# Performance work log

Measured on AMD Instinct MI355X. Metric: run time of the kernel, lower is better.

## Reference

```python
import jax, jax.numpy as jnp
import numpy as np

# SwitchNet f* dims
B = 1024
Nb1, Nw1 = 8, 10          # input: Nb1^2=64 blocks, window 2*Nw1^2=200
Nb2x, Nb2y = 8, 8
Nw2x, Nw2y = 10, 10
R = 16
J1 = Nb1 * Nb1            # 64
K1 = 2 * Nw1 * Nw1        # 200
L1 = Nb2x * Nb2y * R      # 1024
J2 = Nb2x * Nb2y * J1     # 4096
J3 = Nb2x * Nb2y          # 64
K3 = J1 * R               # 1024
L3 = 2 * Nw2x * Nw2y      # 200


def _dm(x, kernel, bias):
    # per-block batched GEMM: x [B, J, K] @ kernel [J, K, L] + bias [1, J, L]
    return jnp.einsum('ijk,jkl->ijl', x, kernel) + bias


def setup_inputs() -> dict:
    key = jax.random.key(0)
    ks = jax.random.split(key, 7)
    u = lambda k, shape: jax.random.uniform(k, shape, dtype=jnp.float32) * 0.01
    return {
        'x': jax.random.normal(ks[0], (B, Nb1 * Nw1 * Nb1 * Nw1, 2), dtype=jnp.float32),
        'k1': u(ks[1], (J1, K1, L1)),
        'b1': u(ks[2], (1, J1, L1)),
        'k2': u(ks[3], (J2, R, R)),
        'b2': u(ks[4], (1, J2, R)),
        'k3': u(ks[5], (J3, K3, L3)),
        'b3': u(ks[6], (1, J3, L3)),
    }


def reference(x, k1, b1, k2, b2, k3, b3):
    bs = x.shape[0]
    # gather input windows: [B, Nb1, Nw1, Nb1, Nw1, 2] -> block-major
    h = x.reshape(bs, Nb1, Nw1, Nb1, Nw1, 2)
    h = h.transpose(0, 1, 3, 2, 4, 5)
    h = h.reshape(bs, J1, K1)
    h = _dm(h, k1, b1)                                   # [B, 64, 1024]
    h = h.reshape(bs, J1, Nb2x * Nb2y, R)
    h = h.transpose(0, 3, 1, 2)                          # [B, r, 64, 64]
    h = h.reshape(bs, J2, R)
    h = _dm(h, k2, b2)                                   # [B, 4096, r]
    h = h.reshape(bs, J3, K3)
    h = _dm(h, k3, b3)                                   # [B, 64, 200]
    h = h.reshape(bs, Nb2x, Nb2y, Nw2x, Nw2y, 2)
    h = h.transpose(0, 1, 3, 2, 4, 5)
    return h.reshape(bs, Nb2x * Nw2x, Nb2y * Nw2y, 2)   # [B, 80, 80, 2]
```

## Files before the change

### kernel.cpp

```cpp
#include <hip/hip_runtime.h>

typedef __attribute__((ext_vector_type(8))) short short8;
typedef __attribute__((ext_vector_type(4))) short bfx4;
typedef __attribute__((ext_vector_type(4))) float floatx4;

__device__ __forceinline__ float bf2f(short u) {
  unsigned int i = ((unsigned int)(unsigned short)u) << 16;
  return __builtin_bit_cast(float, i);
}
__device__ __forceinline__ short f2bf(float f) {
  unsigned int x = __builtin_bit_cast(unsigned int, f);
  x += 0x7fffu + ((x >> 16) & 1u);
  return (short)(x >> 16);
}

__device__ __forceinline__ void gl_lds16(const short* g, short* lds) {
  __builtin_amdgcn_global_load_lds(
      (const __attribute__((address_space(1))) unsigned int*)g,
      (__attribute__((address_space(3))) unsigned int*)lds, 16, 0, 0);
}

#define BC 256


__global__ __launch_bounds__(256) void gather_x(const float* __restrict__ x,
                                                short* __restrict__ hA, int bOffset) {
  int tid = blockIdx.x * 256 + threadIdx.x;
  const int total = 64 * BC * 112;
  if (tid >= total) return;
  int kp2 = tid % 112;
  int rem = tid / 112;
  int b_loc = rem & (BC - 1);
  int j1 = rem / BC;
  unsigned int pair = 0;
  if (kp2 < 100) {
    int wx = kp2 / 10;
    int wy = kp2 - wx * 10;
    int bx = j1 >> 3, by = j1 & 7;
    const float* p = x + (size_t)(bOffset + b_loc) * 12800 +
                     ((size_t)(bx * 800 + wx * 80 + by * 10 + wy)) * 2;
    float2 v = *(const float2*)p;
    pair = ((unsigned int)(unsigned short)f2bf(v.x)) |
           (((unsigned int)(unsigned short)f2bf(v.y)) << 16);
  }
  *(unsigned int*)&hA[rem * 224 + kp2 * 2] = pair;
}

__global__ __launch_bounds__(256) void transpose_k1(const float* __restrict__ k1,
                                                    short* __restrict__ k1t) {
  const int j1 = blockIdx.x;
  const int nBase = blockIdx.y * 64;
  const int kBase = blockIdx.z * 56;
  __shared__ short tr[64][68];
  const int t = threadIdx.x;
  const int nl = t & 63;
  const int ksub = t >> 6;
  const float* src = k1 + (size_t)j1 * 204800 + (size_t)kBase * 1024 + nBase + nl;
#pragma unroll
  for (int pass = 0; pass < 14; ++pass) {
    int kloc = pass * 4 + ksub;
    int k = kBase + kloc;
    tr[nl][kloc] = (k < 200) ? f2bf(src[kloc * 1024]) : (short)0;
  }
  __syncthreads();
  short* dstbase = k1t + ((size_t)j1 * 1024 + nBase) * 224 + kBase;
#pragma unroll
  for (int p = 0; p < 4; ++p) {
    int u = p * 256 + t;
    int row = u >> 4;
    int kq = u & 15;
    if (kq < 14) {
      bfx4 v = *(const bfx4*)&tr[row][kq * 4];
      *(bfx4*)&dstbase[row * 224 + kq * 4] = v;
    }
  }
}

__global__ __launch_bounds__(256) void transpose_k3(const float* __restrict__ k3,
                                                    short* __restrict__ k3t) {
  const int j3 = blockIdx.x;
  const int kBase = blockIdx.y * 128;
  const int nBase = blockIdx.z * 64;
  __shared__ short tr[64][132];
  const int t = threadIdx.x;
  const int nl = t & 63;
  const int ksub = t >> 6;
  const int nGlob = nBase + nl;
  const bool valid = (nGlob < 200);
  const float* src = k3 + (size_t)j3 * 204800 + (size_t)kBase * 200 + nGlob;
#pragma unroll 4
  for (int pass = 0; pass < 32; ++pass) {
    int k = pass * 4 + ksub;
    tr[nl][k] = valid ? f2bf(src[k * 200]) : (short)0;
  }
  __syncthreads();
  short* dstbase = k3t + ((size_t)j3 * 256 + nBase) * 1024 + kBase;
#pragma unroll
  for (int pass = 0; pass < 8; ++pass) {
    int idx = (pass * 256 + t) * 4;
    int row = idx >> 7;
    int koff = idx & 127;
    bfx4 v = *(const bfx4*)&tr[row][koff];
    *(bfx4*)&dstbase[row * 1024 + koff] = v;
  }
}

__global__ __launch_bounds__(256) void gemm_stage1(const short* __restrict__ hA,
                                                   const short* __restrict__ k1t,
                                                   const float* __restrict__ b1,
                                                   short* __restrict__ h1) {
  int bid = (int)blockIdx.x + 8 * (int)blockIdx.y + 16 * (int)blockIdx.z;
  bid = ((bid & 7) << 7) | (bid >> 3);
  const int nBase = (bid & 7) * 128;
  const int mBase = ((bid >> 3) & 1) * 128;
  const int j1 = bid >> 4;
  __shared__ short As[128 * 64];
  __shared__ short Bs[128 * 64];
  const int tid = threadIdx.x;
  const int lane = tid & 63;
  const int wave = tid >> 6;
  const int quad = lane >> 4;
  const int l16 = lane & 15;
  const int wm = wave >> 1, wn = wave & 1;
  const int sRow = tid >> 3;
  const int sCol = ((tid & 7) ^ (sRow & 7)) * 8;
  const short* Aj = hA + (size_t)j1 * BC * 224 + (size_t)(mBase + sRow) * 224 + sCol;
  const short* Bj =
      k1t + (size_t)j1 * 1024 * 224 + (size_t)(nBase + sRow) * 224 + sCol;
  const int tRow = tid >> 2;
  const int tCol = (tid & 3) * 8;
  const short* Ajt =
      hA + (size_t)j1 * BC * 224 + (size_t)(mBase + tRow) * 224 + 192 + tCol;
  const short* Bjt =
      k1t + (size_t)j1 * 1024 * 224 + (size_t)(nBase + tRow) * 224 + 192 + tCol;
  short* ldsA = &As[tid * 8];
  short* ldsB = &Bs[tid * 8];
  floatx4 acc[4][4] = {};

  for (int kk = 0; kk < 192; kk += 64) {
    __syncthreads();
#pragma unroll
    for (int c = 0; c < 4; ++c) {
      gl_lds16(Aj + c * 32 * 224 + kk, ldsA + c * 2048);
      gl_lds16(Bj + c * 32 * 224 + kk, ldsB + c * 2048);
    }
    __syncthreads();
#pragma unroll
    for (int ks = 0; ks < 2; ++ks) {
      short8 af[4], bfv[4];
#pragma unroll
      for (int mt = 0; mt < 4; ++mt) {
        int r = wm * 64 + mt * 16 + l16;
        af[mt] = *(const short8*)&As[r * 64 + ((ks * 4 + quad) ^ (l16 & 7)) * 8];
      }
#pragma unroll
      for (int nt = 0; nt < 4; ++nt) {
        int r = wn * 64 + nt * 16 + l16;
        bfv[nt] = *(const short8*)&Bs[r * 64 + ((ks * 4 + quad) ^ (l16 & 7)) * 8];
      }
#pragma unroll
      for (int mt = 0; mt < 4; ++mt)
#pragma unroll
        for (int nt = 0; nt < 4; ++nt)
          acc[mt][nt] = __builtin_amdgcn_mfma_f32_16x16x32_bf16(af[mt], bfv[nt],
                                                                acc[mt][nt], 0, 0, 0);
    }
  }
  __syncthreads();
  gl_lds16(Ajt, ldsA);
  gl_lds16(Ajt + 64 * 224, ldsA + 2048);
  gl_lds16(Bjt, ldsB);
  gl_lds16(Bjt + 64 * 224, ldsB + 2048);
  __syncthreads();
  {
    short8 af[4], bfv[4];
#pragma unroll
    for (int mt = 0; mt < 4; ++mt)
      af[mt] = *(const short8*)&As[(wm * 64 + mt * 16 + l16) * 32 + quad * 8];
#pragma unroll
    for (int nt = 0; nt < 4; ++nt)
      bfv[nt] = *(const short8*)&Bs[(wn * 64 + nt * 16 + l16) * 32 + quad * 8];
#pragma unroll
    for (int mt = 0; mt < 4; ++mt)
#pragma unroll
      for (int nt = 0; nt < 4; ++nt)
        acc[mt][nt] = __builtin_amdgcn_mfma_f32_16x16x32_bf16(af[mt], bfv[nt],
                                                              acc[mt][nt], 0, 0, 0);
  }
#pragma unroll
  for (int nt = 0; nt < 4; ++nt) {
    int n = nBase + wn * 64 + nt * 16 + l16;
    float bias = b1[j1 * 1024 + n];
    int g = (nBase + wn * 64 + nt * 16) >> 4;
    int nst = ((((g & 15) << 2) | (g >> 4)) << 4) + l16;
#pragma unroll
    for (int mt = 0; mt < 4; ++mt) {
#pragma unroll
      for (int r = 0; r < 4; ++r) {
        int m = mBase + wm * 64 + mt * 16 + quad * 4 + r;
        h1[((size_t)j1 * BC + m) * 1024 + nst] = f2bf(acc[mt][nt][r] + bias);
      }
    }
  }
}

__global__ __launch_bounds__(256) void stage2(const short* __restrict__ h1,
                                              const float* __restrict__ k2,
                                              const float* __restrict__ b2,
                                              short* __restrict__ h2p, int mTot,
                                              int bOff2) {
  int bid = (int)blockIdx.x + 64 * (int)blockIdx.y;
  bid = ((bid & 7) << 7) | (bid >> 3);
  const int j1 = bid >> 4;
  const int bBase = (bid & 15) * 16;
  __shared__ short in_s[16 * 1024];
  const int tid = threadIdx.x;

  const short* inSrc = h1 + ((size_t)j1 * BC + bBase) * 1024 + tid * 8;
  short* inDst = &in_s[tid * 8];
#pragma unroll
  for (int c = 0; c < 8; ++c) gl_lds16(inSrc + c * 2048, inDst + c * 2048);

  const int rem = tid & 63;
  const int oct = tid >> 6;
  const int bh = oct & 1;
  const int ro = oct >> 1;
  const int r = rem >> 2, b2hi = rem & 3;
  const int j2 = r * 256 + j1 * 4 + b2hi;

  float acc[8][8];
  {
    const float* bb = &b2[(size_t)j2 * 16 + ro * 8];
    floatx4 bz0 = *(const floatx4*)bb;
    floatx4 bz1 = *(const floatx4*)(bb + 4);
#pragma unroll
    for (int b = 0; b < 8; ++b)
#pragma unroll
      for (int j = 0; j < 4; ++j) {
        acc[b][j] = bz0[j];
        acc[b][4 + j] = bz1[j];
      }
  }
  __syncthreads();

  const short* inb = &in_s[(bh * 8) * 1024 + b2hi * 16 + r];
  const float* wsrc = &k2[(size_t)j2 * 256 + ro * 8];
#pragma unroll
  for (int k = 0; k < 16; ++k) {
    floatx4 w0 = *(const floatx4*)&wsrc[k * 16];
    floatx4 w1 = *(const floatx4*)&wsrc[k * 16 + 4];
#pragma unroll
    for (int b = 0; b < 8; ++b) {
      float iv = bf2f(inb[b * 1024 + k * 64]);
#pragma unroll
      for (int j = 0; j < 4; ++j) {
        acc[b][j] += iv * w0[j];
        acc[b][4 + j] += iv * w1[j];
      }
    }
  }
  const int j3 = r * 4 + (j1 >> 4);
  const int k3o = (j1 & 15) * 64 + b2hi * 16 + ro * 8;
#pragma unroll
  for (int b = 0; b < 8; ++b) {
    short8 o;
#pragma unroll
    for (int j = 0; j < 8; ++j) o[j] = f2bf(acc[b][j]);
    short* dst =
        h2p + ((size_t)j3 * mTot + bOff2 + bBase + bh * 8 + b) * 1024 + k3o;
    *(short8*)dst = o;
  }
}

__global__ __launch_bounds__(256) void gemm_stage3(const short* __restrict__ h2p,
                                                   const short* __restrict__ k3t,
                                                   const float* __restrict__ b3,
                                                   float* __restrict__ out, int mTot,
                                                   int bOffset) {
  const int gy = (int)gridDim.y;
  int bid = (int)blockIdx.x + 2 * ((int)blockIdx.y + gy * (int)blockIdx.z);
  const int cpx = (gy << 4);
  bid = (bid & 7) * cpx + (bid >> 3);
  const int nBase = (bid & 1) * 128;
  const int rest = bid >> 1;
  const int mBase = (rest & (gy - 1)) * 128;
  const int j3 = rest / gy;
  __shared__ short As[128 * 64];
  __shared__ short Bs[128 * 64];
  const int tid = threadIdx.x;
  const int lane = tid & 63;
  const int wave = tid >> 6;
  const int quad = lane >> 4;
  const int l16 = lane & 15;
  const int wm = wave >> 1, wn = wave & 1;
  const int sRow = tid >> 3;
  const int sCol = ((tid & 7) ^ (sRow & 7)) * 8;
  const short* Aj =
      h2p + (size_t)j3 * mTot * 1024 + (size_t)(mBase + sRow) * 1024 + sCol;
  const short* Bj =
      k3t + (size_t)j3 * 256 * 1024 + (size_t)(nBase + sRow) * 1024 + sCol;
  short* ldsA = &As[tid * 8];
  short* ldsB = &Bs[tid * 8];
  floatx4 acc[4][4] = {};

  for (int kk = 0; kk < 1024; kk += 64) {
    __syncthreads();
#pragma unroll
    for (int c = 0; c < 4; ++c) {
      gl_lds16(Aj + c * 32 * 1024 + kk, ldsA + c * 2048);
      gl_lds16(Bj + c * 32 * 1024 + kk, ldsB + c * 2048);
    }
    __syncthreads();
#pragma unroll
    for (int ks = 0; ks < 2; ++ks) {
      short8 af[4], bfv[4];
#pragma unroll
      for (int mt = 0; mt < 4; ++mt) {
        int r = wm * 64 + mt * 16 + l16;
        af[mt] = *(const short8*)&As[r * 64 + ((ks * 4 + quad) ^ (l16 & 7)) * 8];
      }
#pragma unroll
      for (int nt = 0; nt < 4; ++nt) {
        int r = wn * 64 + nt * 16 + l16;
        bfv[nt] = *(const short8*)&Bs[r * 64 + ((ks * 4 + quad) ^ (l16 & 7)) * 8];
      }
#pragma unroll
      for (int mt = 0; mt < 4; ++mt)
#pragma unroll
        for (int nt = 0; nt < 4; ++nt)
          acc[mt][nt] = __builtin_amdgcn_mfma_f32_16x16x32_bf16(af[mt], bfv[nt],
                                                                acc[mt][nt], 0, 0, 0);
    }
  }
  const int B2x = j3 >> 3, B2y = j3 & 7;
#pragma unroll
  for (int nt = 0; nt < 4; ++nt) {
    int n = nBase + wn * 64 + nt * 16 + l16;
    if (n < 200) {
      float bias = b3[j3 * 200 + n];
      int c = n & 1;
      int t = n >> 1;
      int w2x = t / 10, w2y = t - w2x * 10;
      int orow = B2x * 10 + w2x, ocol = B2y * 10 + w2y;
#pragma unroll
      for (int mt = 0; mt < 4; ++mt) {
#pragma unroll
        for (int r = 0; r < 4; ++r) {
          int m = bOffset + mBase + wm * 64 + mt * 16 + quad * 4 + r;
          out[(((size_t)m * 80 + orow) * 80 + ocol) * 2 + c] = acc[mt][nt][r] + bias;
        }
      }
    }
  }
}

extern "C" void kernel_launch(void* const* d_in, const int* in_sizes, int n_in,
                              void* d_out, int out_size, void* d_ws, size_t ws_size,
                              hipStream_t stream) {
  const float* x = (const float*)d_in[0];
  const float* k1 = (const float*)d_in[1];
  const float* b1 = (const float*)d_in[2];
  const float* k2 = (const float*)d_in[3];
  const float* b2 = (const float*)d_in[4];
  const float* k3 = (const float*)d_in[5];
  const float* b3 = (const float*)d_in[6];
  float* out = (float*)d_out;
  char* ws = (char*)d_ws;

  short* k1t = (short*)(ws);
  short* k3t = (short*)(ws + 29360128);
  short* hA = (short*)(ws + 62914560);
  short* h1c = (short*)(ws + 70254592);
  short* h2p = (short*)(ws + 103809024);

  const bool full = (ws_size >= 238026752ull);
  const int mTot = full ? 1024 : BC;

  transpose_k1<<<dim3(64, 16, 4), 256, 0, stream>>>(k1, k1t);
  transpose_k3<<<dim3(64, 8, 4), 256, 0, stream>>>(k3, k3t);
  for (int c = 0; c < 1024 / BC; ++c) {
    int bOffset = c * BC;
    gather_x<<<(64 * BC * 112) / 256, 256, 0, stream>>>(x, hA, bOffset);
    gemm_stage1<<<dim3(8, BC / 128, 64), 256, 0, stream>>>(hA, k1t, b1, h1c);
    stage2<<<dim3(64, BC / 16), 256, 0, stream>>>(h1c, k2, b2, h2p, mTot,
                                                  full ? bOffset : 0);
    if (!full)
      gemm_stage3<<<dim3(2, BC / 128, 64), 256, 0, stream>>>(h2p, k3t, b3, out, BC,
                                                             bOffset);
  }
  if (full)
    gemm_stage3<<<dim3(2, 1024 / 128, 64), 256, 0, stream>>>(h2p, k3t, b3, out, 1024,
                                                             0);
}
```

Before: 488.0 us.

## Fuse stage-1 GEMM with stage-2 block mixing through shared memory

New measurement: 506.9 us. 3.9% more time.

```diff
diff --git a/kernel.cpp b/kernel.cpp
--- a/kernel.cpp
+++ b/kernel.cpp
@@ -20,18 +20,16 @@
       (__attribute__((address_space(3))) unsigned int*)lds, 16, 0, 0);
 }
 
-#define BC 256
-
-
 __global__ __launch_bounds__(256) void gather_x(const float* __restrict__ x,
-                                                short* __restrict__ hA, int bOffset) {
+                                                short* __restrict__ hA, int bOffset,
+                                                int bShift) {
   int tid = blockIdx.x * 256 + threadIdx.x;
-  const int total = 64 * BC * 112;
+  const int total = (64 << bShift) * 116;
   if (tid >= total) return;
-  int kp2 = tid % 112;
-  int rem = tid / 112;
-  int b_loc = rem & (BC - 1);
-  int j1 = rem / BC;
+  int kp2 = tid % 116;
+  int rem = tid / 116;
+  int b_loc = rem & ((1 << bShift) - 1);
+  int j1 = rem >> bShift;
   unsigned int pair = 0;
   if (kp2 < 100) {
     int wx = kp2 / 10;
@@ -43,7 +41,7 @@
     pair = ((unsigned int)(unsigned short)f2bf(v.x)) |
            (((unsigned int)(unsigned short)f2bf(v.y)) << 16);
   }
-  *(unsigned int*)&hA[rem * 224 + kp2 * 2] = pair;
+  *(unsigned int*)&hA[(size_t)rem * 232 + kp2 * 2] = pair;
 }
 
 __global__ __launch_bounds__(256) void transpose_k1(const float* __restrict__ k1,
@@ -105,170 +103,160 @@
   }
 }
 
-__global__ __launch_bounds__(256) void gemm_stage1(const short* __restrict__ hA,
-                                                   const short* __restrict__ k1t,
-                                                   const float* __restrict__ b1,
-                                                   short* __restrict__ h1) {
-  int bid = (int)blockIdx.x + 8 * (int)blockIdx.y + 16 * (int)blockIdx.z;
-  bid = ((bid & 7) << 7) | (bid >> 3);
-  const int nBase = (bid & 7) * 128;
-  const int mBase = ((bid >> 3) & 1) * 128;
-  const int j1 = bid >> 4;
-  __shared__ short As[128 * 64];
-  __shared__ short Bs[128 * 64];
+__global__ __launch_bounds__(256) void fused12(
+    const short* __restrict__ hA, const short* __restrict__ k1t,
+    const float* __restrict__ b1, const float* __restrict__ k2,
+    const float* __restrict__ b2, short* __restrict__ h2p, int h2pTot,
+    int h2pOff) {
+  const int gx = (int)gridDim.x;
+  int bid = (int)blockIdx.x + gx * (int)blockIdx.y;
+  const int cpx = gx * 8;
+  bid = (bid & 7) * cpx + (bid >> 3);
+  const int j1 = bid / gx;
+  const int mt = bid - j1 * gx;
+  const int BCc = gx * 64;
+
+  __shared__ short lds[31488];
+  short* As = lds;
+  short* Bs = lds + 14848;
+  short* Cs = lds + 23040;
+
   const int tid = threadIdx.x;
   const int lane = tid & 63;
   const int wave = tid >> 6;
   const int quad = lane >> 4;
   const int l16 = lane & 15;
   const int wm = wave >> 1, wn = wave & 1;
+
+  {
+    const short* Asrc = hA + ((size_t)j1 * BCc + mt * 64) * 232 + tid * 8;
+    short* Adst = As + tid * 8;
+#pragma unroll
+    for (int c = 0; c < 8; ++c) gl_lds16(Asrc + c * 2048, Adst + c * 2048);
+  }
+
   const int sRow = tid >> 3;
   const int sCol = ((tid & 7) ^ (sRow & 7)) * 8;
-  const short* Aj = hA + (size_t)j1 * BC * 224 + (size_t)(mBase + sRow) * 224 + sCol;
-  const short* Bj =
-      k1t + (size_t)j1 * 1024 * 224 + (size_t)(nBase + sRow) * 224 + sCol;
+  const short* BjS = k1t + (size_t)j1 * 1024 * 224 + (size_t)sRow * 224 + sCol;
   const int tRow = tid >> 2;
   const int tCol = (tid & 3) * 8;
-  const short* Ajt =
-      hA + (size_t)j1 * BC * 224 + (size_t)(mBase + tRow) * 224 + 192 + tCol;
-  const short* Bjt =
-      k1t + (size_t)j1 * 1024 * 224 + (size_t)(nBase + tRow) * 224 + 192 + tCol;
-  short* ldsA = &As[tid * 8];
+  const short* BjT =
+      k1t + (size_t)j1 * 1024 * 224 + (size_t)tRow * 224 + 192 + tCol;
   short* ldsB = &Bs[tid * 8];
-  floatx4 acc[4][4] = {};
-
-  for (int kk = 0; kk < 192; kk += 64) {
-    __syncthreads();
-#pragma unroll
-    for (int c = 0; c < 4; ++c) {
-      gl_lds16(Aj + c * 32 * 224 + kk, ldsA + c * 2048);
-      gl_lds16(Bj + c * 32 * 224 + kk, ldsB + c * 2048);
-    }
-    __syncthreads();
-#pragma unroll
-    for (int ks = 0; ks < 2; ++ks) {
-      short8 af[4], bfv[4];
-#pragma unroll
-      for (int mt = 0; mt < 4; ++mt) {
-        int r = wm * 64 + mt * 16 + l16;
-        af[mt] = *(const short8*)&As[r * 64 + ((ks * 4 + quad) ^ (l16 & 7)) * 8];
-      }
-#pragma unroll
-      for (int nt = 0; nt < 4; ++nt) {
-        int r = wn * 64 + nt * 16 + l16;
-        bfv[nt] = *(const short8*)&Bs[r * 64 + ((ks * 4 + quad) ^ (l16 & 7)) * 8];
-      }
-#pragma unroll
-      for (int mt = 0; mt < 4; ++mt)
-#pragma unroll
-        for (int nt = 0; nt < 4; ++nt)
-          acc[mt][nt] = __builtin_amdgcn_mfma_f32_16x16x32_bf16(af[mt], bfv[nt],
-                                                                acc[mt][nt], 0, 0, 0);
-    }
-  }
-  __syncthreads();
-  gl_lds16(Ajt, ldsA);
-  gl_lds16(Ajt + 64 * 224, ldsA + 2048);
-  gl_lds16(Bjt, ldsB);
-  gl_lds16(Bjt + 64 * 224, ldsB + 2048);
-  __syncthreads();
-  {
-    short8 af[4], bfv[4];
-#pragma unroll
-    for (int mt = 0; mt < 4; ++mt)
-      af[mt] = *(const short8*)&As[(wm * 64 + mt * 16 + l16) * 32 + quad * 8];
-#pragma unroll
-    for (int nt = 0; nt < 4; ++nt)
-      bfv[nt] = *(const short8*)&Bs[(wn * 64 + nt * 16 + l16) * 32 + quad * 8];
-#pragma unroll
-    for (int mt = 0; mt < 4; ++mt)
-#pragma unroll
-      for (int nt = 0; nt < 4; ++nt)
-        acc[mt][nt] = __builtin_amdgcn_mfma_f32_16x16x32_bf16(af[mt], bfv[nt],
-                                                              acc[mt][nt], 0, 0, 0);
-  }
-#pragma unroll
-  for (int nt = 0; nt < 4; ++nt) {
-    int n = nBase + wn * 64 + nt * 16 + l16;
-    float bias = b1[j1 * 1024 + n];
-    int g = (nBase + wn * 64 + nt * 16) >> 4;
-    int nst = ((((g & 15) << 2) | (g >> 4)) << 4) + l16;
-#pragma unroll
-    for (int mt = 0; mt < 4; ++mt) {
-#pragma unroll
-      for (int r = 0; r < 4; ++r) {
-        int m = mBase + wm * 64 + mt * 16 + quad * 4 + r;
-        h1[((size_t)j1 * BC + m) * 1024 + nst] = f2bf(acc[mt][nt][r] + bias);
-      }
-    }
-  }
-}
-
-__global__ __launch_bounds__(256) void stage2(const short* __restrict__ h1,
-                                              const float* __restrict__ k2,
-                                              const float* __restrict__ b2,
-                                              short* __restrict__ h2p, int mTot,
-                                              int bOff2) {
-  int bid = (int)blockIdx.x + 64 * (int)blockIdx.y;
-  bid = ((bid & 7) << 7) | (bid >> 3);
-  const int j1 = bid >> 4;
-  const int bBase = (bid & 15) * 16;
-  __shared__ short in_s[16 * 1024];
-  const int tid = threadIdx.x;
-
-  const short* inSrc = h1 + ((size_t)j1 * BC + bBase) * 1024 + tid * 8;
-  short* inDst = &in_s[tid * 8];
-#pragma unroll
-  for (int c = 0; c < 8; ++c) gl_lds16(inSrc + c * 2048, inDst + c * 2048);
-
-  const int rem = tid & 63;
-  const int oct = tid >> 6;
-  const int bh = oct & 1;
-  const int ro = oct >> 1;
-  const int r = rem >> 2, b2hi = rem & 3;
-  const int j2 = r * 256 + j1 * 4 + b2hi;
-
-  float acc[8][8];
-  {
-    const float* bb = &b2[(size_t)j2 * 16 + ro * 8];
-    floatx4 bz0 = *(const floatx4*)bb;
-    floatx4 bz1 = *(const floatx4*)(bb + 4);
-#pragma unroll
-    for (int b = 0; b < 8; ++b)
-#pragma unroll
-      for (int j = 0; j < 4; ++j) {
-        acc[b][j] = bz0[j];
-        acc[b][4 + j] = bz1[j];
-      }
-  }
-  __syncthreads();
-
-  const short* inb = &in_s[(bh * 8) * 1024 + b2hi * 16 + r];
-  const float* wsrc = &k2[(size_t)j2 * 256 + ro * 8];
-#pragma unroll
-  for (int k = 0; k < 16; ++k) {
-    floatx4 w0 = *(const floatx4*)&wsrc[k * 16];
-    floatx4 w1 = *(const floatx4*)&wsrc[k * 16 + 4];
-#pragma unroll
-    for (int b = 0; b < 8; ++b) {
-      float iv = bf2f(inb[b * 1024 + k * 64]);
-#pragma unroll
-      for (int j = 0; j < 4; ++j) {
-        acc[b][j] += iv * w0[j];
-        acc[b][4 + j] += iv * w1[j];
-      }
-    }
-  }
-  const int j3 = r * 4 + (j1 >> 4);
-  const int k3o = (j1 & 15) * 64 + b2hi * 16 + ro * 8;
-#pragma unroll
-  for (int b = 0; b < 8; ++b) {
-    short8 o;
-#pragma unroll
-    for (int j = 0; j < 8; ++j) o[j] = f2bf(acc[b][j]);
-    short* dst =
-        h2p + ((size_t)j3 * mTot + bOff2 + bBase + bh * 8 + b) * 1024 + k3o;
-    *(short8*)dst = o;
+
+  const int mg = tid >> 5;
+  const int r2r = (tid >> 1) & 15;
+  const int rh = tid & 1;
+  const int j3 = r2r * 4 + (j1 >> 4);
+  float bacc[8][8];
+
+#pragma unroll 1
+  for (int nc = 0; nc < 8; ++nc) {
+    const int band = nc >> 1;
+    if ((nc & 1) == 0) {
+      const float* bb =
+          b2 + ((size_t)(r2r * 256 + j1 * 4 + band)) * 16 + rh * 8;
+      floatx4 z0 = *(const floatx4*)bb;
+      floatx4 z1 = *(const floatx4*)(bb + 4);
+#pragma unroll
+      for (int m = 0; m < 8; ++m)
+#pragma unroll
+        for (int j = 0; j < 4; ++j) {
+          bacc[m][j] = z0[j];
+          bacc[m][4 + j] = z1[j];
+        }
+    }
+
+    floatx4 acc[2][4] = {};
+    for (int kk = 0; kk < 192; kk += 64) {
+      __syncthreads();
+#pragma unroll
+      for (int c = 0; c < 4; ++c)
+        gl_lds16(BjS + (size_t)(nc * 128 + c * 32) * 224 + kk, ldsB + c * 2048);
+      __syncthreads();
+#pragma unroll
+      for (int ks = 0; ks < 2; ++ks) {
+        short8 af[2], bfv[4];
+#pragma unroll
+        for (int mf = 0; mf < 2; ++mf)
+          af[mf] = *(const short8*)&As[(wm * 32 + mf * 16 + l16) * 232 + kk +
+                                       ks * 32 + quad * 8];
+#pragma unroll
+        for (int nf = 0; nf < 4; ++nf)
+          bfv[nf] = *(const short8*)&Bs[(wn * 64 + nf * 16 + l16) * 64 +
+                                        ((ks * 4 + quad) ^ (l16 & 7)) * 8];
+#pragma unroll
+        for (int mf = 0; mf < 2; ++mf)
+#pragma unroll
+          for (int nf = 0; nf < 4; ++nf)
+            acc[mf][nf] = __builtin_amdgcn_mfma_f32_16x16x32_bf16(
+                af[mf], bfv[nf], acc[mf][nf], 0, 0, 0);
+      }
+    }
+    __syncthreads();
+#pragma unroll
+    for (int c = 0; c < 2; ++c)
+      gl_lds16(BjT + (size_t)(nc * 128 + c * 64) * 224, ldsB + c * 2048);
+    __syncthreads();
+    {
+      short8 af[2], bfv[4];
+#pragma unroll
+      for (int mf = 0; mf < 2; ++mf)
+        af[mf] =
+            *(const short8*)&As[(wm * 32 + mf * 16 + l16) * 232 + 192 + quad * 8];
+#pragma unroll
+      for (int nf = 0; nf < 4; ++nf)
+        bfv[nf] = *(const short8*)&Bs[(wn * 64 + nf * 16 + l16) * 32 + quad * 8];
+#pragma unroll
+      for (int mf = 0; mf < 2; ++mf)
+#pragma unroll
+        for (int nf = 0; nf < 4; ++nf)
+          acc[mf][nf] = __builtin_amdgcn_mfma_f32_16x16x32_bf16(
+              af[mf], bfv[nf], acc[mf][nf], 0, 0, 0);
+    }
+#pragma unroll
+    for (int nf = 0; nf < 4; ++nf) {
+      const int cc = wn * 64 + nf * 16 + l16;
+      const float bias = b1[j1 * 1024 + nc * 128 + cc];
+#pragma unroll
+      for (int mf = 0; mf < 2; ++mf)
+#pragma unroll
+        for (int rr = 0; rr < 4; ++rr)
+          Cs[(wm * 32 + mf * 16 + quad * 4 + rr) * 132 + cc] =
+              f2bf(acc[mf][nf][rr] + bias);
+    }
+    __syncthreads();
+    {
+      const float* wsrc = k2 +
+                          ((size_t)(r2r * 256 + j1 * 4 + band)) * 256 +
+                          ((nc & 1) * 8) * 16 + rh * 8;
+#pragma unroll
+      for (int kl = 0; kl < 8; ++kl) {
+        floatx4 w0 = *(const floatx4*)(wsrc + kl * 16);
+        floatx4 w1 = *(const floatx4*)(wsrc + kl * 16 + 4);
+#pragma unroll
+        for (int m = 0; m < 8; ++m) {
+          float iv = bf2f(Cs[(mg * 8 + m) * 132 + kl * 16 + r2r]);
+#pragma unroll
+          for (int j = 0; j < 4; ++j) {
+            bacc[m][j] += iv * w0[j];
+            bacc[m][4 + j] += iv * w1[j];
+          }
+        }
+      }
+    }
+    if (nc & 1) {
+      const int k3o = (j1 & 15) * 64 + band * 16 + rh * 8;
+#pragma unroll
+      for (int m = 0; m < 8; ++m) {
+        short8 o;
+#pragma unroll
+        for (int j = 0; j < 8; ++j) o[j] = f2bf(bacc[m][j]);
+        *(short8*)&h2p[((size_t)j3 * h2pTot + h2pOff + mt * 64 + mg * 8 + m) *
+                           1024 +
+                       k3o] = o;
+      }
+    }
   }
 }
 
@@ -370,25 +358,25 @@
   short* k1t = (short*)(ws);
   short* k3t = (short*)(ws + 29360128);
   short* hA = (short*)(ws + 62914560);
-  short* h1c = (short*)(ws + 70254592);
-  short* h2p = (short*)(ws + 103809024);
-
-  const bool full = (ws_size >= 238026752ull);
-  const int mTot = full ? 1024 : BC;
+
+  const bool full = (ws_size >= 227540992ull);
 
   transpose_k1<<<dim3(64, 16, 4), 256, 0, stream>>>(k1, k1t);
   transpose_k3<<<dim3(64, 8, 4), 256, 0, stream>>>(k3, k3t);
-  for (int c = 0; c < 1024 / BC; ++c) {
-    int bOffset = c * BC;
-    gather_x<<<(64 * BC * 112) / 256, 256, 0, stream>>>(x, hA, bOffset);
-    gemm_stage1<<<dim3(8, BC / 128, 64), 256, 0, stream>>>(hA, k1t, b1, h1c);
-    stage2<<<dim3(64, BC / 16), 256, 0, stream>>>(h1c, k2, b2, h2p, mTot,
-                                                  full ? bOffset : 0);
-    if (!full)
-      gemm_stage3<<<dim3(2, BC / 128, 64), 256, 0, stream>>>(h2p, k3t, b3, out, BC,
-                                                             bOffset);
-  }
-  if (full)
-    gemm_stage3<<<dim3(2, 1024 / 128, 64), 256, 0, stream>>>(h2p, k3t, b3, out, 1024,
-                                                             0);
-}
+
+  if (full) {
+    short* h2p = (short*)(ws + 62914560 + 30408704);
+    gather_x<<<(64 * 1024 * 116) / 256, 256, 0, stream>>>(x, hA, 0, 10);
+    fused12<<<dim3(16, 64), 256, 0, stream>>>(hA, k1t, b1, k2, b2, h2p, 1024, 0);
+    gemm_stage3<<<dim3(2, 8, 64), 256, 0, stream>>>(h2p, k3t, b3, out, 1024, 0);
+  } else {
+    short* h2p = (short*)(ws + 62914560 + 7602176);
+    for (int c = 0; c < 4; ++c) {
+      int bOffset = c * 256;
+      gather_x<<<(64 * 256 * 116) / 256, 256, 0, stream>>>(x, hA, bOffset, 8);
+      fused12<<<dim3(4, 64), 256, 0, stream>>>(hA, k1t, b1, k2, b2, h2p, 256, 0);
+      gemm_stage3<<<dim3(2, 2, 64), 256, 0, stream>>>(h2p, k3t, b3, out, 256,
+                                                      bOffset);
+    }
+  }
+}
```
